# Performance work log

Measured on AMD Instinct MI355X. Metric: run time of the kernel, lower is better.

## Reference

```python
import jax, jax.numpy as jnp
import numpy as np

OUT_H, OUT_W = 7, 7
SPATIAL_SCALE = 0.25
SAMPLING_RATIO = 2  # samples per bin per axis (static; torchvision default -1 is data-dependent)


def _axis_coords(start, bin_size, n_bins, s):
    # sample coordinates along one axis for every roi: [K, n_bins*s]
    i = jnp.arange(n_bins * s, dtype=start.dtype)
    t = (i // s) + ((i % s) + 0.5) / s  # fractional bin position
    return start[:, None] + bin_size[:, None] * t[None, :]


def _corner_setup(c, size):
    # torchvision bilinear_interpolate boundary handling (aligned=False legacy)
    valid = (c >= -1.0) & (c <= size)
    cc = jnp.maximum(c, 0.0)
    low = jnp.minimum(jnp.floor(cc).astype(jnp.int32), size - 1)
    high = jnp.minimum(low + 1, size - 1)
    frac = cc - low.astype(cc.dtype)  # when low==high the frac weight is irrelevant
    return low, high, frac, valid


def roi_align(feat, rois, out_h, out_w, spatial_scale, s):
    B, C, H, W = feat.shape
    K = rois.shape[0]
    b = rois[:, 0].astype(jnp.int32)
    x1 = rois[:, 1] * spatial_scale
    y1 = rois[:, 2] * spatial_scale
    x2 = rois[:, 3] * spatial_scale
    y2 = rois[:, 4] * spatial_scale
    roi_w = jnp.maximum(x2 - x1, 1.0)
    roi_h = jnp.maximum(y2 - y1, 1.0)
    bin_w = roi_w / out_w
    bin_h = roi_h / out_h

    ys = _axis_coords(y1, bin_h, out_h, s)  # [K, out_h*s]
    xs = _axis_coords(x1, bin_w, out_w, s)  # [K, out_w*s]

    yl, yh, fy, vy = _corner_setup(ys, H)
    xl, xh, fx, vx = _corner_setup(xs, W)

    hy, ly = 1.0 - fy, fy  # [K, Py]
    hx, lx = 1.0 - fx, fx  # [K, Px]

    bi = b[:, None, None]

    def gather(yi, xi):
        # advanced indexing -> [K, Py, Px, C]
        return feat[bi, :, yi[:, :, None], xi[:, None, :]]

    def w(a, bb):
        return (a[:, :, None] * bb[:, None, :])[..., None]  # [K,Py,Px,1]

    v = (w(hy, hx) * gather(yl, xl)
         + w(hy, lx) * gather(yl, xh)
         + w(ly, hx) * gather(yh, xl)
         + w(ly, lx) * gather(yh, xh))

    mask = (vy[:, :, None] & vx[:, None, :]).astype(feat.dtype)[..., None]
    v = v * mask  # out-of-bounds samples contribute 0

    # average over the s*s samples in each bin
    v = v.reshape(K, out_h, s, out_w, s, C).mean(axis=(2, 4))  # [K,out_h,out_w,C]
    return jnp.transpose(v, (0, 3, 1, 2))  # [K, C, out_h, out_w]


def setup_inputs() -> dict:
    key = jax.random.key(0)
    k1, k2, k3, k4, k5 = jax.random.split(key, 5)
    B, C, H, W = 4, 256, 128, 128
    K = 1024
    img = W / SPATIAL_SCALE  # 512 image-space extent
    feat = jax.random.normal(k1, (B, C, H, W), dtype=jnp.float32)
    bidx = jax.random.randint(k2, (K,), 0, B).astype(jnp.float32)
    x1 = jax.random.uniform(k3, (K,), minval=0.0, maxval=img * 0.75)
    y1 = jax.random.uniform(k4, (K,), minval=0.0, maxval=img * 0.75)
    wh = jax.random.uniform(k5, (K, 2), minval=8.0, maxval=img * 0.25)
    x2 = jnp.minimum(x1 + wh[:, 0], img - 1.0)
    y2 = jnp.minimum(y1 + wh[:, 1], img - 1.0)
    rois = jnp.stack([bidx, x1, y1, x2, y2], axis=1)
    return {"input": feat, "rois": rois}


def reference(input, rois):
    return roi_align(input, rois, OUT_H, OUT_W, SPATIAL_SCALE, SAMPLING_RATIO)
```

## Files before the change

### kernel.cpp

```cpp
#include <hip/hip_runtime.h>


typedef unsigned short u16;
typedef unsigned int u32;

#define FW 128
#define FHW 16384
#define NC 256
#define NB 4
#define HALF_C 128
#define OUT_PER_HALF 6272
#define TILE_P 129

static __device__ __forceinline__ float bfhi(u32 v) {
  return __uint_as_float(v & 0xFFFF0000u);
}
static __device__ __forceinline__ float bflo(u32 v) {
  return __uint_as_float(v << 16);
}

__global__ __launch_bounds__(256) void repack_kernel(const float* __restrict__ feat,
                                                     u16* __restrict__ ws) {
  __shared__ u16 tile[64][66];
  int hw0 = blockIdx.x * 64;
  int c0  = blockIdx.y * 64;
  int b   = blockIdx.z;
  const float* src = feat + (size_t)b * NC * FHW;
  int t   = threadIdx.x;
  int lhw = t & 63;
  int lc  = t >> 6;
#pragma unroll
  for (int i = 0; i < 16; ++i) {
    int c = lc + i * 4;
    float v = src[(size_t)(c0 + c) * FHW + hw0 + lhw];
    u32 u = __float_as_uint(v);
    u += 0x7FFFu + ((u >> 16) & 1u);
    tile[lhw][c] = (u16)(u >> 16);
  }
  __syncthreads();
  u16* dst = ws + (size_t)b * FHW * NC;
  int c2 = (t & 31) * 2;
  int r0 = t >> 5;
#pragma unroll
  for (int i = 0; i < 8; ++i) {
    int r = r0 + i * 8;
    u32 val = *(const u32*)&tile[r][c2];
    *(u32*)&dst[(size_t)(hw0 + r) * NC + c0 + c2] = val;
  }
}

__global__ __launch_bounds__(256) void gather_kernel(const u16* __restrict__ ws,
                                                     const float* __restrict__ rois,
                                                     float* __restrict__ out) {
  __shared__ float tile[49][TILE_P];
  int bid    = blockIdx.x;
  int k      = bid >> 1;
  int half   = bid & 1;
  int t      = threadIdx.x;
  int slot   = t >> 4;
  int lane16 = t & 15;
  int cl     = lane16 * 8;

  int   b  = (int)rois[k * 5 + 0];
  float x1 = rois[k * 5 + 1] * 0.25f;
  float y1 = rois[k * 5 + 2] * 0.25f;
  float x2 = rois[k * 5 + 3] * 0.25f;
  float y2 = rois[k * 5 + 4] * 0.25f;
  float bw = fmaxf(x2 - x1, 1.0f) * (1.0f / 7.0f);
  float bh = fmaxf(y2 - y1, 1.0f) * (1.0f / 7.0f);

  const u16* plane = ws + (size_t)b * FHW * NC + half * HALF_C + cl;
  const int s0 = slot ? 3 * slot + 1 : 0;
  const int nb = slot ? 3 : 4;

  float acc[4][8];
#pragma unroll
  for (int i = 0; i < 4; ++i)
#pragma unroll
    for (int ch = 0; ch < 8; ++ch) acc[i][ch] = 0.0f;

#pragma unroll
  for (int i = 0; i < 4; ++i) {
    if (i < nb) {
      int s  = s0 + i;
      int ph = s / 7, pw = s - ph * 7;

      int xl[2], xh[2]; float fx[2]; bool vx[2];
#pragma unroll
      for (int ix = 0; ix < 2; ++ix) {
        float xx = x1 + bw * ((float)pw + (ix ? 0.75f : 0.25f));
        vx[ix] = (xx >= -1.0f) && (xx <= 128.0f);
        float xc = fmaxf(xx, 0.0f);
        int l = min((int)xc, 127);
        xl[ix] = l; xh[ix] = min(l + 1, 127); fx[ix] = xc - (float)l;
      }
      int yl[2], yh[2]; float fy[2]; bool vy[2];
#pragma unroll
      for (int iy = 0; iy < 2; ++iy) {
        float yy = y1 + bh * ((float)ph + (iy ? 0.75f : 0.25f));
        vy[iy] = (yy >= -1.0f) && (yy <= 128.0f);
        float yc = fmaxf(yy, 0.0f);
        int l = min((int)yc, 127);
        yl[iy] = l; yh[iy] = min(l + 1, 127); fy[iy] = yc - (float)l;
      }

#pragma unroll
      for (int iy = 0; iy < 2; ++iy) {
#pragma unroll
        for (int ix = 0; ix < 2; ++ix) {
          if (vy[iy] && vx[ix]) {
            float ly_ = fy[iy], hy = 1.0f - ly_;
            float lx_ = fx[ix], hx = 1.0f - lx_;
            float w00 = hy * hx, w01 = hy * lx_, w10 = ly_ * hx, w11 = ly_ * lx_;
            const uint4 v00 = *(const uint4*)(plane + (yl[iy] * FW + xl[ix]) * NC);
            const uint4 v01 = *(const uint4*)(plane + (yl[iy] * FW + xh[ix]) * NC);
            const uint4 v10 = *(const uint4*)(plane + (yh[iy] * FW + xl[ix]) * NC);
            const uint4 v11 = *(const uint4*)(plane + (yh[iy] * FW + xh[ix]) * NC);
            acc[i][0] += w00 * bflo(v00.x) + w01 * bflo(v01.x) + w10 * bflo(v10.x) + w11 * bflo(v11.x);
            acc[i][1] += w00 * bfhi(v00.x) + w01 * bfhi(v01.x) + w10 * bfhi(v10.x) + w11 * bfhi(v11.x);
            acc[i][2] += w00 * bflo(v00.y) + w01 * bflo(v01.y) + w10 * bflo(v10.y) + w11 * bflo(v11.y);
            acc[i][3] += w00 * bfhi(v00.y) + w01 * bfhi(v01.y) + w10 * bfhi(v10.y) + w11 * bfhi(v11.y);
            acc[i][4] += w00 * bflo(v00.z) + w01 * bflo(v01.z) + w10 * bflo(v10.z) + w11 * bflo(v11.z);
            acc[i][5] += w00 * bfhi(v00.z) + w01 * bfhi(v01.z) + w10 * bfhi(v10.z) + w11 * bfhi(v11.z);
            acc[i][6] += w00 * bflo(v00.w) + w01 * bflo(v01.w) + w10 * bflo(v10.w) + w11 * bflo(v11.w);
            acc[i][7] += w00 * bfhi(v00.w) + w01 * bfhi(v01.w) + w10 * bfhi(v10.w) + w11 * bfhi(v11.w);
          }
        }
      }
    }
  }

#pragma unroll
  for (int i = 0; i < 4; ++i) {
    if (i < nb) {
      int s = s0 + i;
#pragma unroll
      for (int ch = 0; ch < 8; ++ch) tile[s][cl + ch] = acc[i][ch] * 0.25f;
    }
  }
  __syncthreads();

  float* o = out + (size_t)k * (NC * 49) + half * OUT_PER_HALF;
#pragma unroll
  for (int i = 0; i < 25; ++i) {
    int f = t + i * 256;
    if (f < OUT_PER_HALF) {
      int c = f / 49;
      int s = f - c * 49;
      o[f] = tile[s][c];
    }
  }
}

__global__ __launch_bounds__(256) void ROIAlign_direct(const float* __restrict__ feat,
                                                       const float* __restrict__ rois,
                                                       float* __restrict__ out, int n) {
  int o = blockIdx.x * 256 + threadIdx.x;
  if (o >= n) return;
  int pw = o % 7;
  int t1 = o / 7;
  int ph = t1 % 7;
  int t2 = t1 / 7;
  int c = t2 & 255;
  int k = t2 >> 8;

  int rb = k * 5;
  int b = (int)rois[rb + 0];
  float x1 = rois[rb + 1] * 0.25f, y1 = rois[rb + 2] * 0.25f;
  float x2 = rois[rb + 3] * 0.25f, y2 = rois[rb + 4] * 0.25f;
  float bw = fmaxf(x2 - x1, 1.0f) / 7.0f;
  float bh = fmaxf(y2 - y1, 1.0f) / 7.0f;

  int xl[2], xh[2]; float fx[2]; bool vx[2];
#pragma unroll
  for (int ix = 0; ix < 2; ++ix) {
    float xx = x1 + bw * ((float)pw + (ix ? 0.75f : 0.25f));
    vx[ix] = (xx >= -1.0f) && (xx <= 128.0f);
    float xc = fmaxf(xx, 0.0f);
    int l = min((int)xc, 127);
    xl[ix] = l; xh[ix] = min(l + 1, 127); fx[ix] = xc - (float)l;
  }
  int yl[2], yh[2]; float fy[2]; bool vy[2];
#pragma unroll
  for (int iy = 0; iy < 2; ++iy) {
    float yy = y1 + bh * ((float)ph + (iy ? 0.75f : 0.25f));
    vy[iy] = (yy >= -1.0f) && (yy <= 128.0f);
    float yc = fmaxf(yy, 0.0f);
    int l = min((int)yc, 127);
    yl[iy] = l; yh[iy] = min(l + 1, 127); fy[iy] = yc - (float)l;
  }
  const int plane = (b * 256 + c) << 14;
  float acc = 0.0f;
#pragma unroll
  for (int iy = 0; iy < 2; ++iy) {
    int ro0 = plane + (yl[iy] << 7);
    int ro1 = plane + (yh[iy] << 7);
#pragma unroll
    for (int ix = 0; ix < 2; ++ix) {
      if (vy[iy] && vx[ix]) {
        float ly_ = fy[iy], hy = 1.0f - ly_;
        float lx_ = fx[ix], hx = 1.0f - lx_;
        acc += hy * (hx * feat[ro0 + xl[ix]] + lx_ * feat[ro0 + xh[ix]]) +
               ly_ * (hx * feat[ro1 + xl[ix]] + lx_ * feat[ro1 + xh[ix]]);
      }
    }
  }
  out[o] = acc * 0.25f;
}

extern "C" void kernel_launch(void* const* d_in, const int* in_sizes, int n_in,
                              void* d_out, int out_size, void* d_ws, size_t ws_size,
                              hipStream_t stream) {
  const float* feat = (const float*)d_in[0];
  const float* rois = (const float*)d_in[1];
  float* out = (float*)d_out;
  int K = out_size / (NC * 49);
  size_t need = (size_t)NB * FHW * NC * sizeof(u16);
  if (ws_size >= need) {
    repack_kernel<<<dim3(FHW / 64, NC / 64, NB), 256, 0, stream>>>(feat, (u16*)d_ws);
    gather_kernel<<<dim3(2 * K), 256, 0, stream>>>((const u16*)d_ws, rois, out);
  } else {
    int n = out_size;
    ROIAlign_direct<<<(n + 255) / 256, 256, 0, stream>>>(feat, rois, out, n);
  }
}
```

Before: 55.65 us.

## Sort ROIs by batch and position and remap blocks per XCD for L2 locality

Adds a single-block bitonic sort that orders ROIs by batch index and coarse top-left position, then maps gather blocks so that each XCD processes a contiguous run of spatially nearby ROIs. The goal is more reuse of the repacked bf16 feature map in each XCD's L2 and fewer redundant HBM fetches. It adds an extra kernel launch and a serial sort with many barriers, and hardcodes K=1024 ROIs.

```diff
diff --git a/kernel.cpp b/kernel.cpp
--- a/kernel.cpp
+++ b/kernel.cpp
@@ -3,6 +3,7 @@
 
 typedef unsigned short u16;
 typedef unsigned int u32;
+typedef unsigned long long u64;
 
 #define FW 128
 #define FHW 16384
@@ -11,6 +12,8 @@
 #define HALF_C 128
 #define OUT_PER_HALF 6272
 #define TILE_P 129
+#define KROIS 1024
+#define WS_REPACK_BYTES ((size_t)NB * FHW * NC * sizeof(u16))
 
 static __device__ __forceinline__ float bfhi(u32 v) {
   return __uint_as_float(v & 0xFFFF0000u);
@@ -49,13 +52,44 @@
   }
 }
 
+__global__ __launch_bounds__(1024) void sort_rois_kernel(const float* __restrict__ rois,
+                                                         u32* __restrict__ perm) {
+  __shared__ u64 keys[KROIS];
+  int t = threadIdx.x;
+  {
+    int b   = (int)rois[t * 5 + 0];
+    float y = rois[t * 5 + 2] * 0.25f;
+    float x = rois[t * 5 + 1] * 0.25f;
+    int cy = min(max((int)y, 0), 127);
+    int cx = min(max((int)x, 0), 127);
+    keys[t] = ((u64)b << 32) | ((u64)(cy >> 1) << 24) | ((u64)(cx >> 1) << 16) | (u32)t;
+  }
+  __syncthreads();
+  for (int size = 2; size <= KROIS; size <<= 1) {
+    for (int stride = size >> 1; stride > 0; stride >>= 1) {
+      int p = t ^ stride;
+      if (p > t) {
+        bool up = ((t & size) == 0);
+        u64 a = keys[t], bb = keys[p];
+        if ((a > bb) == up) { keys[t] = bb; keys[p] = a; }
+      }
+      __syncthreads();
+    }
+  }
+  perm[t] = (u32)(keys[t] & 0xFFFFu);
+}
+
 __global__ __launch_bounds__(256) void gather_kernel(const u16* __restrict__ ws,
                                                      const float* __restrict__ rois,
+                                                     const u32* __restrict__ perm,
                                                      float* __restrict__ out) {
   __shared__ float tile[49][TILE_P];
   int bid    = blockIdx.x;
-  int k      = bid >> 1;
-  int half   = bid & 1;
+  int xcd    = bid & 7;
+  int j      = bid >> 3;
+  int lin    = xcd * ((2 * KROIS) >> 3) + j;
+  int k      = perm[lin >> 1];
+  int half   = lin & 1;
   int t      = threadIdx.x;
   int slot   = t >> 4;
   int lane16 = t & 15;
@@ -214,13 +248,15 @@
   const float* feat = (const float*)d_in[0];
   const float* rois = (const float*)d_in[1];
   float* out = (float*)d_out;
-  int K = out_size / (NC * 49);
-  size_t need = (size_t)NB * FHW * NC * sizeof(u16);
+  int n = out_size;
+  size_t need = WS_REPACK_BYTES + KROIS * sizeof(u32);
   if (ws_size >= need) {
-    repack_kernel<<<dim3(FHW / 64, NC / 64, NB), 256, 0, stream>>>(feat, (u16*)d_ws);
-    gather_kernel<<<dim3(2 * K), 256, 0, stream>>>((const u16*)d_ws, rois, out);
+    u16* ws_feat = (u16*)d_ws;
+    u32* perm    = (u32*)((char*)d_ws + WS_REPACK_BYTES);
+    repack_kernel<<<dim3(FHW / 64, NC / 64, NB), 256, 0, stream>>>(feat, ws_feat);
+    sort_rois_kernel<<<1, KROIS, 0, stream>>>(rois, perm);
+    gather_kernel<<<dim3(2 * KROIS), 256, 0, stream>>>(ws_feat, rois, perm, out);
   } else {
-    int n = out_size;
     ROIAlign_direct<<<(n + 255) / 256, 256, 0, stream>>>(feat, rois, out, n);
   }
 }
```

After: 58.28 us. 1.05x slower.
